# Kernel tuning notes

Measured on AMD Instinct MI355X. Metric: run time of the kernel, lower is better.

## Reference

```python
import jax, jax.numpy as jnp
import numpy as np
import math

D_MODEL = 1024
NUM_HEADS = 16
D_K = D_MODEL // NUM_HEADS
THETA = 10000.0
NEG_INF = 1.0e6  # module uses -1e6, not -inf


def _rope_tables(seq_len):
    pair_idx = jnp.arange(0, D_K, 2, dtype=jnp.float32)
    inv_freq = 1.0 / (THETA ** (pair_idx / D_K))
    pos = jnp.arange(seq_len, dtype=jnp.float32)
    angles = jnp.outer(pos, inv_freq)  # (S, D_K//2)
    return jnp.cos(angles), jnp.sin(angles)


def _apply_rope(x, cos, sin):
    # x: (B, H, S, D_K); cos/sin: (S, D_K//2)
    xe = x[..., 0::2]
    xo = x[..., 1::2]
    oe = xe * cos - xo * sin
    oo = xe * sin + xo * cos
    return jnp.stack([oe, oo], axis=-1).reshape(x.shape)


def setup_inputs() -> dict:
    key = jax.random.key(0)
    k0, k1, k2, k3, k4 = jax.random.split(key, 5)
    B, S = 2, 2048
    x = jax.random.normal(k0, (B, S, D_MODEL), dtype=jnp.float32)
    scale = 0.02
    wq = jax.random.normal(k1, (D_MODEL, D_MODEL), dtype=jnp.float32) * scale
    wk = jax.random.normal(k2, (D_MODEL, D_MODEL), dtype=jnp.float32) * scale
    wv = jax.random.normal(k3, (D_MODEL, D_MODEL), dtype=jnp.float32) * scale
    wo = jax.random.normal(k4, (D_MODEL, D_MODEL), dtype=jnp.float32) * scale
    return {"x": x, "wq": wq, "wk": wk, "wv": wv, "wo": wo}


def reference(x, wq, wk, wv, wo):
    B, S, _ = x.shape
    q = x @ wq.T
    k = x @ wk.T
    v = x @ wv.T
    # (B, S, H, d_k) -> (B, H, S, d_k)
    q = q.reshape(B, S, NUM_HEADS, D_K).transpose(0, 2, 1, 3)
    k = k.reshape(B, S, NUM_HEADS, D_K).transpose(0, 2, 1, 3)
    v = v.reshape(B, S, NUM_HEADS, D_K).transpose(0, 2, 1, 3)
    cos, sin = _rope_tables(S)
    q = _apply_rope(q, cos, sin)
    k = _apply_rope(k, cos, sin)
    scores = jnp.einsum("bhqd,bhkd->bhqk", q, k) / math.sqrt(D_K)
    causal = jnp.tril(jnp.ones((S, S), dtype=bool))
    scores = jnp.where(causal, scores, -NEG_INF)
    attn = jax.nn.softmax(scores, axis=-1)
    out = jnp.einsum("bhqk,bhkd->bhqd", attn, v)
    out = out.transpose(0, 2, 1, 3).reshape(B, S, D_MODEL)
    return out @ wo.T
```

## Files before the change

kernel.cpp:

```cpp
#include <hip/hip_runtime.h>

typedef __attribute__((ext_vector_type(8))) __bf16 bf16x8;
typedef __attribute__((ext_vector_type(4))) float f32x4;
typedef __attribute__((ext_vector_type(8))) unsigned short u16x8;

#define MFMA(a, b, c) __builtin_amdgcn_mfma_f32_16x16x32_bf16((a), (b), (c), 0, 0, 0)
#define LOG2E 1.44269504088896340736f

__device__ __forceinline__ float b2f(unsigned short u) {
    union { unsigned int i; float f; } v; v.i = ((unsigned int)u) << 16; return v.f;
}
__device__ __forceinline__ unsigned short f2bf(float f) {
    union { float f; unsigned int i; } v; v.f = f;
    unsigned int u = v.i;
    return (unsigned short)((u + 0x7fffu + ((u >> 16) & 1u)) >> 16);
}

__device__ __forceinline__ void gl_lds16(const void* g, void* l) {
    __builtin_amdgcn_global_load_lds(
        (const __attribute__((address_space(1))) void*)g,
        (__attribute__((address_space(3))) void*)l,
        16, 0, 0);
}

__global__ __launch_bounds__(256) void cvt_all(const float* __restrict__ x,
                                               const float* __restrict__ wq,
                                               const float* __restrict__ wk,
                                               const float* __restrict__ wv,
                                               const float* __restrict__ wo,
                                               unsigned short* __restrict__ xb,
                                               unsigned short* __restrict__ wqb,
                                               unsigned short* __restrict__ wkb,
                                               unsigned short* __restrict__ wvb,
                                               unsigned short* __restrict__ wob) {
    int id = blockIdx.x * 256 + threadIdx.x;
    const float* src; unsigned short* dst; size_t off;
    if (id < 524288)      { src = x;  dst = xb;  off = (size_t)id * 8; }
    else if (id < 655360) { src = wq; dst = wqb; off = (size_t)(id - 524288) * 8; }
    else if (id < 786432) { src = wk; dst = wkb; off = (size_t)(id - 655360) * 8; }
    else if (id < 917504) { src = wv; dst = wvb; off = (size_t)(id - 786432) * 8; }
    else                  { src = wo; dst = wob; off = (size_t)(id - 917504) * 8; }
    float4 a = *(const float4*)(src + off);
    float4 b = *(const float4*)(src + off + 4);
    u16x8 o;
    o[0] = f2bf(a.x); o[1] = f2bf(a.y); o[2] = f2bf(a.z); o[3] = f2bf(a.w);
    o[4] = f2bf(b.x); o[5] = f2bf(b.y); o[6] = f2bf(b.z); o[7] = f2bf(b.w);
    *(u16x8*)(dst + off) = o;
}

template <typename OutT>
__device__ __forceinline__ void gemm128_bt(const unsigned short* __restrict__ A,
                                           const unsigned short* __restrict__ B,
                                           OutT* __restrict__ C,
                                           int m0, int n0,
                                           unsigned short* As, unsigned short* Bs) {
    const int tid = threadIdx.x;
    const int w = tid >> 6, lane = tid & 63;
    const int quad = lane >> 4, l15 = lane & 15;
    const int wm = w & 1, wn = w >> 1;

    f32x4 acc[4][4];
#pragma unroll
    for (int mt = 0; mt < 4; ++mt)
#pragma unroll
        for (int nt = 0; nt < 4; ++nt) acc[mt][nt] = f32x4{0.f, 0.f, 0.f, 0.f};

    for (int k0 = 0; k0 < 1024; k0 += 32) {
        __syncthreads();
#pragma unroll
        for (int i = 0; i < 2; ++i) {
            int L = (w * 2 + i) * 64 + lane;
            int r = L >> 2;
            int c = (L & 3) ^ ((r >> 1) & 3);
            gl_lds16(A + (size_t)(m0 + r) * 1024 + k0 + c * 8, As + L * 8);
            gl_lds16(B + (size_t)(n0 + r) * 1024 + k0 + c * 8, Bs + L * 8);
        }
        __syncthreads();

        bf16x8 af[4], bfr[4];
#pragma unroll
        for (int mt = 0; mt < 4; ++mt) {
            int row = wm * 64 + mt * 16 + l15;
            af[mt] = *(const bf16x8*)(As + row * 32 + (quad ^ ((row >> 1) & 3)) * 8);
        }
#pragma unroll
        for (int nt = 0; nt < 4; ++nt) {
            int row = wn * 64 + nt * 16 + l15;
            bfr[nt] = *(const bf16x8*)(Bs + row * 32 + (quad ^ ((row >> 1) & 3)) * 8);
        }
#pragma unroll
        for (int mt = 0; mt < 4; ++mt)
#pragma unroll
            for (int nt = 0; nt < 4; ++nt)
                acc[mt][nt] = MFMA(af[mt], bfr[nt], acc[mt][nt]);
    }

#pragma unroll
    for (int mt = 0; mt < 4; ++mt) {
        int grow = m0 + wm * 64 + mt * 16 + quad * 4;
#pragma unroll
        for (int nt = 0; nt < 4; ++nt) {
            int gcol = n0 + wn * 64 + nt * 16 + l15;
#pragma unroll
            for (int r = 0; r < 4; ++r) {
                float val = acc[mt][nt][r];
                if constexpr (sizeof(OutT) == 2)
                    C[(size_t)(grow + r) * 1024 + gcol] = (OutT)f2bf(val);
                else
                    C[(size_t)(grow + r) * 1024 + gcol] = (OutT)val;
            }
        }
    }
}

__global__ __launch_bounds__(256) void gemm_qkv(const unsigned short* __restrict__ X,
                                                const unsigned short* __restrict__ Wq,
                                                const unsigned short* __restrict__ Wk,
                                                const unsigned short* __restrict__ Wv,
                                                unsigned short* __restrict__ Qo,
                                                unsigned short* __restrict__ Ko,
                                                unsigned short* __restrict__ Vo) {
    __shared__ unsigned short As[128 * 32];
    __shared__ unsigned short Bs[128 * 32];
    int m0 = blockIdx.x * 128;
    int sel = blockIdx.y >> 3;
    int n0 = (blockIdx.y & 7) * 128;
    const unsigned short* B = (sel == 0) ? Wq : ((sel == 1) ? Wk : Wv);
    unsigned short* C = (sel == 0) ? Qo : ((sel == 1) ? Ko : Vo);
    gemm128_bt<unsigned short>(X, B, C, m0, n0, As, Bs);
}

__global__ __launch_bounds__(256) void gemm_out(const unsigned short* __restrict__ A,
                                                const unsigned short* __restrict__ Wo,
                                                float* __restrict__ C) {
    __shared__ unsigned short As[128 * 32];
    __shared__ unsigned short Bs[128 * 32];
    gemm128_bt<float>(A, Wo, C, blockIdx.x * 128, blockIdx.y * 128, As, Bs);
}

__global__ __launch_bounds__(256) void rope_qk(unsigned short* __restrict__ Q,
                                               unsigned short* __restrict__ K) {
    int id = blockIdx.x * 256 + threadIdx.x;
    int tsel = id >> 21;
    int rgt = id & 0x1FFFFF;
    int row = rgt >> 9;
    int p = rgt & 511;
    int pp = p & 31;
    int col = (p >> 5) * 64 + pp * 2;
    float pos = (float)(row & 2047);
    float inv_freq = exp2f(-0.41524101186092029f * (float)pp);
    float ang = pos * inv_freq;
    float sn, cs;
    sincosf(ang, &sn, &cs);
    unsigned short* buf = tsel ? K : Q;
    float scale = tsel ? 1.0f : (0.125f * LOG2E);
    size_t base = (size_t)row * 1024 + col;
    float xe = b2f(buf[base]), xo = b2f(buf[base + 1]);
    buf[base]     = f2bf((xe * cs - xo * sn) * scale);
    buf[base + 1] = f2bf((xe * sn + xo * cs) * scale);
}

__global__ __launch_bounds__(256) void transpose_v(const unsigned short* __restrict__ V,
                                                   unsigned short* __restrict__ Vt) {
    int st = blockIdx.x, bh = blockIdx.y;
    int b = bh >> 4, h = bh & 15;
    __shared__ unsigned short t[64][72];
    int tid = threadIdx.x;
#pragma unroll
    for (int it = 0; it < 2; ++it) {
        int idx = it * 256 + tid;
        int sl = idx >> 3, dg = (idx & 7) * 8;
        u16x8 val = *(const u16x8*)(V + (size_t)(b * 2048 + st * 64 + sl) * 1024 + h * 64 + dg);
#pragma unroll
        for (int j = 0; j < 8; ++j) t[sl][dg + j] = val[j];
    }
    __syncthreads();
#pragma unroll
    for (int it = 0; it < 2; ++it) {
        int idx = it * 256 + tid;
        int dl = idx >> 3, sg = (idx & 7) * 8;
        u16x8 v;
#pragma unroll
        for (int j = 0; j < 8; ++j) v[j] = t[sg + j][dl];
        *(u16x8*)(Vt + (size_t)(bh * 64 + dl) * 2048 + st * 64 + sg) = v;
    }
}

__global__ __launch_bounds__(256) void flash_attn(const unsigned short* __restrict__ Q,
                                                  const unsigned short* __restrict__ Kb,
                                                  const unsigned short* __restrict__ Vt,
                                                  unsigned short* __restrict__ O) {
    int id = blockIdx.x;
    int xcd = id & 7, rem = id >> 3;
    int qt = 31 - (rem & 31);
    int bh = xcd + 8 * (rem >> 5);
    int b = bh >> 4, h = bh & 15;
    int tid = threadIdx.x, w = tid >> 6, lane = tid & 63;
    int quad = lane >> 4, l15 = lane & 15;
    int qrow0 = b * 2048 + qt * 64 + w * 16;
    int qpos0 = qt * 64 + w * 16;

    __shared__ unsigned short Ks[2][64 * 64];
    __shared__ unsigned short Vs[2][64 * 64];
    __shared__ unsigned short Ps[4][16 * 72];

    bf16x8 qf0, qf1;
    {
        const unsigned short* qp = Q + (size_t)(qrow0 + l15) * 1024 + h * 64 + quad * 8;
        qf0 = *(const bf16x8*)qp;
        qf1 = *(const bf16x8*)(qp + 32);
    }

    int L0 = w * 128 + lane;
    int L1 = L0 + 64;
    int r0 = L0 >> 3, c0s = (L0 & 7) ^ (r0 & 7);
    int r1 = L1 >> 3, c1s = (L1 & 7) ^ (r1 & 7);
    const unsigned short* Kg0 = Kb + (size_t)(b * 2048 + r0) * 1024 + h * 64 + c0s * 8;
    const unsigned short* Kg1 = Kb + (size_t)(b * 2048 + r1) * 1024 + h * 64 + c1s * 8;
    const unsigned short* Vg0 = Vt + (size_t)(bh * 64 + r0) * 2048 + c0s * 8;
    const unsigned short* Vg1 = Vt + (size_t)(bh * 64 + r1) * 2048 + c1s * 8;

    f32x4 accO[4];
#pragma unroll
    for (int nt = 0; nt < 4; ++nt) accO[nt] = f32x4{0.f, 0.f, 0.f, 0.f};
    float lsum[4] = {0.f, 0.f, 0.f, 0.f};

    int nkb = qt + 1;

    {
        gl_lds16(Kg0, Ks[0] + L0 * 8);
        gl_lds16(Kg1, Ks[0] + L1 * 8);
        gl_lds16(Vg0, Vs[0] + L0 * 8);
        gl_lds16(Vg1, Vs[0] + L1 * 8);
    }

    for (int kb = 0; kb < nkb; ++kb) {
        __syncthreads();
        if (kb + 1 < nkb) {
            int bi = (kb + 1) & 1;
            size_t ko = (size_t)(kb + 1) * 64 * 1024;
            size_t vo = (size_t)(kb + 1) * 64;
            gl_lds16(Kg0 + ko, Ks[bi] + L0 * 8);
            gl_lds16(Kg1 + ko, Ks[bi] + L1 * 8);
            gl_lds16(Vg0 + vo, Vs[bi] + L0 * 8);
            gl_lds16(Vg1 + vo, Vs[bi] + L1 * 8);
        }
        const unsigned short* Kc = Ks[kb & 1];
        const unsigned short* Vc = Vs[kb & 1];

        if (kb * 64 <= qpos0 + 15) {
            f32x4 s[4];
#pragma unroll
            for (int nt = 0; nt < 4; ++nt) {
                int row = nt * 16 + l15;
                int cof = (quad ^ (row & 7)) * 8;
                bf16x8 kf0 = *(const bf16x8*)(Kc + row * 64 + cof);
                bf16x8 kf1 = *(const bf16x8*)(Kc + row * 64 + (cof ^ 32));
                f32x4 z = f32x4{0.f, 0.f, 0.f, 0.f};
                s[nt] = MFMA(qf0, kf0, z);
                s[nt] = MFMA(qf1, kf1, s[nt]);
            }
            unsigned short* Pw = Ps[w];
#pragma unroll
            for (int nt = 0; nt < 4; ++nt) {
                int kpos = kb * 64 + nt * 16 + l15;
#pragma unroll
                for (int r = 0; r < 4; ++r) {
                    int qpos = qpos0 + quad * 4 + r;
                    float e = exp2f(s[nt][r]);
                    e = (kpos > qpos) ? 0.f : e;
                    lsum[r] += e;
                    Pw[(quad * 4 + r) * 72 + nt * 16 + l15] = f2bf(e);
                }
            }
            __asm__ volatile("s_waitcnt lgkmcnt(0)" ::: "memory");
            bf16x8 pf0 = *(const bf16x8*)(Pw + l15 * 72 + quad * 8);
            bf16x8 pf1 = *(const bf16x8*)(Pw + l15 * 72 + 32 + quad * 8);
#pragma unroll
            for (int nt = 0; nt < 4; ++nt) {
                int row = nt * 16 + l15;
                int cof = (quad ^ (row & 7)) * 8;
                bf16x8 vf0 = *(const bf16x8*)(Vc + row * 64 + cof);
                bf16x8 vf1 = *(const bf16x8*)(Vc + row * 64 + (cof ^ 32));
                accO[nt] = MFMA(pf0, vf0, accO[nt]);
                accO[nt] = MFMA(pf1, vf1, accO[nt]);
            }
        }
    }
#pragma unroll
    for (int off = 1; off < 16; off <<= 1)
#pragma unroll
        for (int r = 0; r < 4; ++r) lsum[r] += __shfl_xor(lsum[r], off);
    float inv[4];
#pragma unroll
    for (int r = 0; r < 4; ++r) inv[r] = 1.0f / lsum[r];
#pragma unroll
    for (int nt = 0; nt < 4; ++nt)
#pragma unroll
        for (int r = 0; r < 4; ++r)
            O[(size_t)(qrow0 + quad * 4 + r) * 1024 + h * 64 + nt * 16 + l15] =
                f2bf(accO[nt][r] * inv[r]);
}

extern "C" void kernel_launch(void* const* d_in, const int* in_sizes, int n_in,
                              void* d_out, int out_size, void* d_ws, size_t ws_size,
                              hipStream_t stream) {
    (void)in_sizes; (void)n_in; (void)out_size; (void)ws_size;
    const float* x  = (const float*)d_in[0];
    const float* wq = (const float*)d_in[1];
    const float* wk = (const float*)d_in[2];
    const float* wv = (const float*)d_in[3];
    const float* wo = (const float*)d_in[4];
    float* out = (float*)d_out;

    const size_t T = (size_t)4096 * 1024;
    const size_t W = (size_t)1024 * 1024;
    unsigned short* Q   = (unsigned short*)d_ws;
    unsigned short* K   = Q + T;
    unsigned short* Vt  = K + T;
    unsigned short* Vr  = Vt + T;
    unsigned short* AO  = Vr + T;
    unsigned short* xb  = AO + T;
    unsigned short* wqb = xb + T;
    unsigned short* wkb = wqb + W;
    unsigned short* wvb = wkb + W;
    unsigned short* wob = wvb + W;

    cvt_all    <<<dim3(4096),   256, 0, stream>>>(x, wq, wk, wv, wo, xb, wqb, wkb, wvb, wob);
    gemm_qkv   <<<dim3(32, 24), 256, 0, stream>>>(xb, wqb, wkb, wvb, Q, K, Vr);
    rope_qk    <<<dim3(16384),  256, 0, stream>>>(Q, K);
    transpose_v<<<dim3(32, 32), 256, 0, stream>>>(Vr, Vt);
    flash_attn <<<dim3(1024),   256, 0, stream>>>(Q, K, Vt, AO);
    gemm_out   <<<dim3(32, 8),  256, 0, stream>>>(AO, wob, out);
}
```

Baseline: 214.7 us.

## Fuse V transpose into QKV GEMM, use fp16 P·V and MFMA row sums

The V projection is now computed as Wv·X^T, so the QKV GEMM writes V already transposed (in fp16, with a new ldc) and the separate transpose kernel and its buffer are removed. In flash attention, P is packed with cvt_pkrtz to fp16 and the P·V products use fp16 MFMA. Row sums are accumulated with an MFMA against a ones vector instead of scalar adds plus shuffles. The key loop is split so the causal mask is applied only on the diagonal block, which drops the per-block branch. Storing V and P in fp16 changes precision, and the round-toward-zero conversion adds a small bias.

```diff
diff --git a/kernel.cpp b/kernel.cpp
--- a/kernel.cpp
+++ b/kernel.cpp
@@ -1,10 +1,13 @@
 #include <hip/hip_runtime.h>
 
 typedef __attribute__((ext_vector_type(8))) __bf16 bf16x8;
+typedef __attribute__((ext_vector_type(8))) _Float16 f16x8;
+typedef __attribute__((ext_vector_type(2))) _Float16 f16x2;
 typedef __attribute__((ext_vector_type(4))) float f32x4;
 typedef __attribute__((ext_vector_type(8))) unsigned short u16x8;
 
-#define MFMA(a, b, c) __builtin_amdgcn_mfma_f32_16x16x32_bf16((a), (b), (c), 0, 0, 0)
+#define MFMA_BF16(a, b, c) __builtin_amdgcn_mfma_f32_16x16x32_bf16((a), (b), (c), 0, 0, 0)
+#define MFMA_F16(a, b, c)  __builtin_amdgcn_mfma_f32_16x16x32_f16((a), (b), (c), 0, 0, 0)
 #define LOG2E 1.44269504088896340736f
 
 __device__ __forceinline__ float b2f(unsigned short u) {
@@ -48,11 +51,11 @@
     *(u16x8*)(dst + off) = o;
 }
 
-template <typename OutT>
+template <int MODE>
 __device__ __forceinline__ void gemm128_bt(const unsigned short* __restrict__ A,
                                            const unsigned short* __restrict__ B,
-                                           OutT* __restrict__ C,
-                                           int m0, int n0,
+                                           void* __restrict__ Cv,
+                                           int m0, int n0, int ldc,
                                            unsigned short* As, unsigned short* Bs) {
     const int tid = threadIdx.x;
     const int w = tid >> 6, lane = tid & 63;
@@ -92,7 +95,7 @@
         for (int mt = 0; mt < 4; ++mt)
 #pragma unroll
             for (int nt = 0; nt < 4; ++nt)
-                acc[mt][nt] = MFMA(af[mt], bfr[nt], acc[mt][nt]);
+                acc[mt][nt] = MFMA_BF16(af[mt], bfr[nt], acc[mt][nt]);
     }
 
 #pragma unroll
@@ -104,10 +107,15 @@
 #pragma unroll
             for (int r = 0; r < 4; ++r) {
                 float val = acc[mt][nt][r];
-                if constexpr (sizeof(OutT) == 2)
-                    C[(size_t)(grow + r) * 1024 + gcol] = (OutT)f2bf(val);
-                else
-                    C[(size_t)(grow + r) * 1024 + gcol] = (OutT)val;
+                size_t idx = (size_t)(grow + r) * ldc + gcol;
+                if constexpr (MODE == 0) {
+                    ((unsigned short*)Cv)[idx] = f2bf(val);
+                } else if constexpr (MODE == 1) {
+                    ((float*)Cv)[idx] = val;
+                } else {
+                    _Float16 hv = (_Float16)val;
+                    ((unsigned short*)Cv)[idx] = __builtin_bit_cast(unsigned short, hv);
+                }
             }
         }
     }
@@ -119,15 +127,22 @@
                                                 const unsigned short* __restrict__ Wv,
                                                 unsigned short* __restrict__ Qo,
                                                 unsigned short* __restrict__ Ko,
-                                                unsigned short* __restrict__ Vo) {
+                                                unsigned short* __restrict__ Vt) {
     __shared__ unsigned short As[128 * 32];
     __shared__ unsigned short Bs[128 * 32];
-    int m0 = blockIdx.x * 128;
-    int sel = blockIdx.y >> 3;
-    int n0 = (blockIdx.y & 7) * 128;
-    const unsigned short* B = (sel == 0) ? Wq : ((sel == 1) ? Wk : Wv);
-    unsigned short* C = (sel == 0) ? Qo : ((sel == 1) ? Ko : Vo);
-    gemm128_bt<unsigned short>(X, B, C, m0, n0, As, Bs);
+    int y = blockIdx.y;
+    if (y < 16) {
+        int sel = y >> 3;
+        int m0 = blockIdx.x * 128;
+        int n0 = (y & 7) * 128;
+        const unsigned short* B = sel ? Wk : Wq;
+        unsigned short* C = sel ? Ko : Qo;
+        gemm128_bt<0>(X, B, C, m0, n0, 1024, As, Bs);
+    } else {
+        int m0 = (y & 7) * 128;
+        int n0 = blockIdx.x * 128;
+        gemm128_bt<2>(Wv, X, Vt, m0, n0, 4096, As, Bs);
+    }
 }
 
 __global__ __launch_bounds__(256) void gemm_out(const unsigned short* __restrict__ A,
@@ -135,7 +150,7 @@
                                                 float* __restrict__ C) {
     __shared__ unsigned short As[128 * 32];
     __shared__ unsigned short Bs[128 * 32];
-    gemm128_bt<float>(A, Wo, C, blockIdx.x * 128, blockIdx.y * 128, As, Bs);
+    gemm128_bt<1>(A, Wo, C, blockIdx.x * 128, blockIdx.y * 128, 1024, As, Bs);
 }
 
 __global__ __launch_bounds__(256) void rope_qk(unsigned short* __restrict__ Q,
@@ -160,31 +175,61 @@
     buf[base + 1] = f2bf((xe * sn + xo * cs) * scale);
 }
 
-__global__ __launch_bounds__(256) void transpose_v(const unsigned short* __restrict__ V,
-                                                   unsigned short* __restrict__ Vt) {
-    int st = blockIdx.x, bh = blockIdx.y;
-    int b = bh >> 4, h = bh & 15;
-    __shared__ unsigned short t[64][72];
-    int tid = threadIdx.x;
-#pragma unroll
-    for (int it = 0; it < 2; ++it) {
-        int idx = it * 256 + tid;
-        int sl = idx >> 3, dg = (idx & 7) * 8;
-        u16x8 val = *(const u16x8*)(V + (size_t)(b * 2048 + st * 64 + sl) * 1024 + h * 64 + dg);
-#pragma unroll
-        for (int j = 0; j < 8; ++j) t[sl][dg + j] = val[j];
-    }
-    __syncthreads();
-#pragma unroll
-    for (int it = 0; it < 2; ++it) {
-        int idx = it * 256 + tid;
-        int dl = idx >> 3, sg = (idx & 7) * 8;
-        u16x8 v;
-#pragma unroll
-        for (int j = 0; j < 8; ++j) v[j] = t[sg + j][dl];
-        *(u16x8*)(Vt + (size_t)(bh * 64 + dl) * 2048 + st * 64 + sg) = v;
-    }
-}
+#define FLASH_BODY(KB, MASKED)                                                          \
+    {                                                                                   \
+        const int kb_ = (KB);                                                           \
+        const unsigned short* Kc = Ks[kb_ & 1];                                         \
+        const unsigned short* Vc = Vs[kb_ & 1];                                         \
+        f32x4 s[4];                                                                     \
+        _Pragma("unroll")                                                               \
+        for (int nt = 0; nt < 4; ++nt) {                                                \
+            int row = nt * 16 + l15;                                                    \
+            int cof = (quad ^ (row & 7)) * 8;                                           \
+            bf16x8 kf0 = *(const bf16x8*)(Kc + row * 64 + cof);                         \
+            bf16x8 kf1 = *(const bf16x8*)(Kc + row * 64 + (cof ^ 32));                  \
+            f32x4 z = f32x4{0.f, 0.f, 0.f, 0.f};                                        \
+            s[nt] = MFMA_BF16(qf0, kf0, z);                                             \
+            s[nt] = MFMA_BF16(qf1, kf1, s[nt]);                                         \
+        }                                                                               \
+        unsigned short* Pw = Ps[w];                                                     \
+        _Pragma("unroll")                                                               \
+        for (int nt = 0; nt < 4; ++nt) {                                                \
+            float e[4];                                                                 \
+            _Pragma("unroll")                                                           \
+            for (int r = 0; r < 4; ++r) {                                               \
+                float ev = exp2f(s[nt][r]);                                             \
+                if (MASKED) {                                                           \
+                    int kpos = kb_ * 64 + nt * 16 + l15;                                \
+                    int qpos = qpos0 + quad * 4 + r;                                    \
+                    ev = (kpos > qpos) ? 0.f : ev;                                      \
+                }                                                                       \
+                e[r] = ev;                                                              \
+            }                                                                           \
+            unsigned pk01 = __builtin_bit_cast(unsigned,                                \
+                                __builtin_amdgcn_cvt_pkrtz(e[0], e[1]));                \
+            unsigned pk23 = __builtin_bit_cast(unsigned,                                \
+                                __builtin_amdgcn_cvt_pkrtz(e[2], e[3]));                \
+            int col = nt * 16 + l15;                                                    \
+            Pw[(quad * 4 + 0) * 72 + col] = (unsigned short)pk01;                       \
+            Pw[(quad * 4 + 1) * 72 + col] = (unsigned short)(pk01 >> 16);               \
+            Pw[(quad * 4 + 2) * 72 + col] = (unsigned short)pk23;                       \
+            Pw[(quad * 4 + 3) * 72 + col] = (unsigned short)(pk23 >> 16);               \
+        }                                                                               \
+        __asm__ volatile("s_waitcnt lgkmcnt(0)" ::: "memory");                          \
+        f16x8 pf0 = *(const f16x8*)(Pw + l15 * 72 + quad * 8);                          \
+        f16x8 pf1 = *(const f16x8*)(Pw + l15 * 72 + 32 + quad * 8);                     \
+        lacc = MFMA_F16(pf0, ones, lacc);                                               \
+        lacc = MFMA_F16(pf1, ones, lacc);                                               \
+        _Pragma("unroll")                                                               \
+        for (int nt = 0; nt < 4; ++nt) {                                                \
+            int row = nt * 16 + l15;                                                    \
+            int cof = (quad ^ (row & 7)) * 8;                                           \
+            f16x8 vf0 = *(const f16x8*)(Vc + row * 64 + cof);                           \
+            f16x8 vf1 = *(const f16x8*)(Vc + row * 64 + (cof ^ 32));                    \
+            accO[nt] = MFMA_F16(pf0, vf0, accO[nt]);                                    \
+            accO[nt] = MFMA_F16(pf1, vf1, accO[nt]);                                    \
+        }                                                                               \
+    }
 
 __global__ __launch_bounds__(256) void flash_attn(const unsigned short* __restrict__ Q,
                                                   const unsigned short* __restrict__ Kb,
@@ -210,6 +255,9 @@
         qf0 = *(const bf16x8*)qp;
         qf1 = *(const bf16x8*)(qp + 32);
     }
+    f16x8 ones;
+#pragma unroll
+    for (int j = 0; j < 8; ++j) ones[j] = (_Float16)1.0f;
 
     int L0 = w * 128 + lane;
     int L1 = L0 + 64;
@@ -217,83 +265,36 @@
     int r1 = L1 >> 3, c1s = (L1 & 7) ^ (r1 & 7);
     const unsigned short* Kg0 = Kb + (size_t)(b * 2048 + r0) * 1024 + h * 64 + c0s * 8;
     const unsigned short* Kg1 = Kb + (size_t)(b * 2048 + r1) * 1024 + h * 64 + c1s * 8;
-    const unsigned short* Vg0 = Vt + (size_t)(bh * 64 + r0) * 2048 + c0s * 8;
-    const unsigned short* Vg1 = Vt + (size_t)(bh * 64 + r1) * 2048 + c1s * 8;
+    const unsigned short* Vg0 = Vt + (size_t)(h * 64 + r0) * 4096 + b * 2048 + c0s * 8;
+    const unsigned short* Vg1 = Vt + (size_t)(h * 64 + r1) * 4096 + b * 2048 + c1s * 8;
 
     f32x4 accO[4];
 #pragma unroll
     for (int nt = 0; nt < 4; ++nt) accO[nt] = f32x4{0.f, 0.f, 0.f, 0.f};
-    float lsum[4] = {0.f, 0.f, 0.f, 0.f};
-
-    int nkb = qt + 1;
-
-    {
-        gl_lds16(Kg0, Ks[0] + L0 * 8);
-        gl_lds16(Kg1, Ks[0] + L1 * 8);
-        gl_lds16(Vg0, Vs[0] + L0 * 8);
-        gl_lds16(Vg1, Vs[0] + L1 * 8);
-    }
-
-    for (int kb = 0; kb < nkb; ++kb) {
+    f32x4 lacc = f32x4{0.f, 0.f, 0.f, 0.f};
+
+    gl_lds16(Kg0, Ks[0] + L0 * 8);
+    gl_lds16(Kg1, Ks[0] + L1 * 8);
+    gl_lds16(Vg0, Vs[0] + L0 * 8);
+    gl_lds16(Vg1, Vs[0] + L1 * 8);
+
+    for (int kb = 0; kb < qt; ++kb) {
         __syncthreads();
-        if (kb + 1 < nkb) {
-            int bi = (kb + 1) & 1;
-            size_t ko = (size_t)(kb + 1) * 64 * 1024;
-            size_t vo = (size_t)(kb + 1) * 64;
-            gl_lds16(Kg0 + ko, Ks[bi] + L0 * 8);
-            gl_lds16(Kg1 + ko, Ks[bi] + L1 * 8);
-            gl_lds16(Vg0 + vo, Vs[bi] + L0 * 8);
-            gl_lds16(Vg1 + vo, Vs[bi] + L1 * 8);
-        }
-        const unsigned short* Kc = Ks[kb & 1];
-        const unsigned short* Vc = Vs[kb & 1];
-
-        if (kb * 64 <= qpos0 + 15) {
-            f32x4 s[4];
-#pragma unroll
-            for (int nt = 0; nt < 4; ++nt) {
-                int row = nt * 16 + l15;
-                int cof = (quad ^ (row & 7)) * 8;
-                bf16x8 kf0 = *(const bf16x8*)(Kc + row * 64 + cof);
-                bf16x8 kf1 = *(const bf16x8*)(Kc + row * 64 + (cof ^ 32));
-                f32x4 z = f32x4{0.f, 0.f, 0.f, 0.f};
-                s[nt] = MFMA(qf0, kf0, z);
-                s[nt] = MFMA(qf1, kf1, s[nt]);
-            }
-            unsigned short* Pw = Ps[w];
-#pragma unroll
-            for (int nt = 0; nt < 4; ++nt) {
-                int kpos = kb * 64 + nt * 16 + l15;
-#pragma unroll
-                for (int r = 0; r < 4; ++r) {
-                    int qpos = qpos0 + quad * 4 + r;
-                    float e = exp2f(s[nt][r]);
-                    e = (kpos > qpos) ? 0.f : e;
-                    lsum[r] += e;
-                    Pw[(quad * 4 + r) * 72 + nt * 16 + l15] = f2bf(e);
-                }
-            }
-            __asm__ volatile("s_waitcnt lgkmcnt(0)" ::: "memory");
-            bf16x8 pf0 = *(const bf16x8*)(Pw + l15 * 72 + quad * 8);
-            bf16x8 pf1 = *(const bf16x8*)(Pw + l15 * 72 + 32 + quad * 8);
-#pragma unroll
-            for (int nt = 0; nt < 4; ++nt) {
-                int row = nt * 16 + l15;
-                int cof = (quad ^ (row & 7)) * 8;
-                bf16x8 vf0 = *(const bf16x8*)(Vc + row * 64 + cof);
-                bf16x8 vf1 = *(const bf16x8*)(Vc + row * 64 + (cof ^ 32));
-                accO[nt] = MFMA(pf0, vf0, accO[nt]);
-                accO[nt] = MFMA(pf1, vf1, accO[nt]);
-            }
-        }
-    }
-#pragma unroll
-    for (int off = 1; off < 16; off <<= 1)
-#pragma unroll
-        for (int r = 0; r < 4; ++r) lsum[r] += __shfl_xor(lsum[r], off);
+        int bi = (kb + 1) & 1;
+        size_t ko = (size_t)(kb + 1) * 64 * 1024;
+        size_t vo = (size_t)(kb + 1) * 64;
+        gl_lds16(Kg0 + ko, Ks[bi] + L0 * 8);
+        gl_lds16(Kg1 + ko, Ks[bi] + L1 * 8);
+        gl_lds16(Vg0 + vo, Vs[bi] + L0 * 8);
+        gl_lds16(Vg1 + vo, Vs[bi] + L1 * 8);
+        FLASH_BODY(kb, 0)
+    }
+    __syncthreads();
+    FLASH_BODY(qt, 1)
+
     float inv[4];
 #pragma unroll
-    for (int r = 0; r < 4; ++r) inv[r] = 1.0f / lsum[r];
+    for (int r = 0; r < 4; ++r) inv[r] = 1.0f / lacc[r];
 #pragma unroll
     for (int nt = 0; nt < 4; ++nt)
 #pragma unroll
@@ -318,18 +319,16 @@
     unsigned short* Q   = (unsigned short*)d_ws;
     unsigned short* K   = Q + T;
     unsigned short* Vt  = K + T;
-    unsigned short* Vr  = Vt + T;
-    unsigned short* AO  = Vr + T;
+    unsigned short* AO  = Vt + T;
     unsigned short* xb  = AO + T;
     unsigned short* wqb = xb + T;
     unsigned short* wkb = wqb + W;
     unsigned short* wvb = wkb + W;
     unsigned short* wob = wvb + W;
 
-    cvt_all    <<<dim3(4096),   256, 0, stream>>>(x, wq, wk, wv, wo, xb, wqb, wkb, wvb, wob);
-    gemm_qkv   <<<dim3(32, 24), 256, 0, stream>>>(xb, wqb, wkb, wvb, Q, K, Vr);
-    rope_qk    <<<dim3(16384),  256, 0, stream>>>(Q, K);
-    transpose_v<<<dim3(32, 32), 256, 0, stream>>>(Vr, Vt);
-    flash_attn <<<dim3(1024),   256, 0, stream>>>(Q, K, Vt, AO);
-    gemm_out   <<<dim3(32, 8),  256, 0, stream>>>(AO, wob, out);
-}
+    cvt_all  <<<dim3(4096),   256, 0, stream>>>(x, wq, wk, wv, wo, xb, wqb, wkb, wvb, wob);
+    gemm_qkv <<<dim3(32, 24), 256, 0, stream>>>(xb, wqb, wkb, wvb, Q, K, Vt);
+    rope_qk  <<<dim3(16384),  256, 0, stream>>>(Q, K);
+    flash_attn<<<dim3(1024),  256, 0, stream>>>(Q, K, Vt, AO);
+    gemm_out <<<dim3(32, 8),  256, 0, stream>>>(AO, wob, out);
+}
```

Measured after the change: 198.0 us. -7.8%, faster.
